# Kernel optimization log

Measured on AMD Instinct MI355X. Metric: run time of the kernel, lower is better.

The kernel has to match this reference:

```python
import jax, jax.numpy as jnp
import numpy as np

N, D_IN, D_OUT = 500000, 128, 128
DROP_P = 0.5


def setup_inputs() -> dict:
    key = jax.random.key(0)
    k1, k2, k3, k4 = jax.random.split(key, 4)
    x = jax.random.normal(k1, (N, D_IN), dtype=jnp.float32)
    weight = jax.random.normal(k2, (D_IN, D_OUT), dtype=jnp.float32)
    support = jax.random.normal(k3, (D_OUT, D_OUT), dtype=jnp.float32)
    # inverted-dropout mask: Bernoulli(keep=1-p) scaled by 1/(1-p), matching F.dropout in training mode
    keep = 1.0 - DROP_P
    u = jax.random.uniform(k4, (N, D_IN), dtype=jnp.float32)
    drop_mask = (u < keep).astype(jnp.float32) / keep
    return {"x": x, "weight": weight, "support": support, "drop_mask": drop_mask}


def reference(x, weight, support, drop_mask):
    # training-mode dropout (deterministic mask), dense transform, right-multiply by support, ReLU
    xd = x * drop_mask                      # [N, D_IN]
    xw = jnp.matmul(xd, weight)             # [N, D_OUT]
    out = jnp.matmul(xw, support)           # [N, D_OUT]
    return jax.nn.relu(out)
```

## Files before the change

kernel.cpp:

```cpp
#include <hip/hip_runtime.h>
#include <hip/hip_bf16.h>


#define D 128
#define LDS_PITCH 136

typedef __attribute__((ext_vector_type(8))) short short8;
typedef __attribute__((ext_vector_type(4))) float f32x4;

__device__ __forceinline__ short f2bf(float f) {
    union { __hip_bfloat16 h; short s; } u;
    u.h = __float2bfloat16(f);
    return u.s;
}

__global__ void wprod_kernel(const float* __restrict__ weight,
                             const float* __restrict__ support,
                             unsigned short* __restrict__ wt) {
    __shared__ float wrow[D];
    const int i = blockIdx.x;
    const int j = threadIdx.x;
    wrow[j] = weight[i * D + j];
    __syncthreads();
    float acc = 0.f;
#pragma unroll 8
    for (int k = 0; k < D; ++k)
        acc = fmaf(wrow[k], support[k * D + j], acc);
    union { __hip_bfloat16 h; unsigned short s; } u;
    u.h = __float2bfloat16(acc);
    wt[(size_t)j * D + i] = u.s;
}

__global__ __launch_bounds__(256, 4) void gcn_fused(
    const float* __restrict__ x, const float* __restrict__ mask,
    const unsigned short* __restrict__ wt, float* __restrict__ out,
    int nslabs) {
    __shared__ __align__(16) unsigned short lw[D * LDS_PITCH];

    const uint4* src = reinterpret_cast<const uint4*>(wt);
    for (int c = threadIdx.x; c < 2048; c += 256) {
        const int n = c >> 4;
        const int kc = (c & 15) << 3;
        *reinterpret_cast<uint4*>(&lw[n * LDS_PITCH + kc]) = src[c];
    }
    __syncthreads();

    const int lane = threadIdx.x & 63;
    const int m = lane & 15;
    const int quad = lane >> 4;

    const int wave = (blockIdx.x * blockDim.x + threadIdx.x) >> 6;
    const int nwaves = (gridDim.x * blockDim.x) >> 6;

    for (int s = wave; s < nslabs; s += nwaves) {
        const float* xr = x + ((size_t)s * 16 + m) * D + quad * 8;
        const float* mr = mask + ((size_t)s * 16 + m) * D + quad * 8;

        short8 a[4];
#pragma unroll
        for (int kk = 0; kk < 4; ++kk) {
            f32x4 x0 = *reinterpret_cast<const f32x4*>(xr + kk * 32);
            f32x4 x1 = *reinterpret_cast<const f32x4*>(xr + kk * 32 + 4);
            f32x4 m0 = *reinterpret_cast<const f32x4*>(mr + kk * 32);
            f32x4 m1 = *reinterpret_cast<const f32x4*>(mr + kk * 32 + 4);
            f32x4 p0 = x0 * m0;
            f32x4 p1 = x1 * m1;
            short8 v;
            v[0] = f2bf(p0[0]); v[1] = f2bf(p0[1]);
            v[2] = f2bf(p0[2]); v[3] = f2bf(p0[3]);
            v[4] = f2bf(p1[0]); v[5] = f2bf(p1[1]);
            v[6] = f2bf(p1[2]); v[7] = f2bf(p1[3]);
            a[kk] = v;
        }

        float* orow = out + (size_t)s * 16 * D;
#pragma unroll
        for (int n = 0; n < 8; ++n) {
            f32x4 acc = {0.f, 0.f, 0.f, 0.f};
#pragma unroll
            for (int kk = 0; kk < 4; ++kk) {
                const short8 b = *reinterpret_cast<const short8*>(
                    &lw[(n * 16 + m) * LDS_PITCH + kk * 32 + quad * 8]);
                acc = __builtin_amdgcn_mfma_f32_16x16x32_bf16(a[kk], b, acc, 0, 0, 0);
            }
#pragma unroll
            for (int r = 0; r < 4; ++r) {
                const float v = acc[r];
                orow[(quad * 4 + r) * D + n * 16 + m] = v > 0.f ? v : 0.f;
            }
        }
    }
}

extern "C" void kernel_launch(void* const* d_in, const int* in_sizes, int n_in,
                              void* d_out, int out_size, void* d_ws, size_t ws_size,
                              hipStream_t stream) {
    const float* x = (const float*)d_in[0];
    const float* weight = (const float*)d_in[1];
    const float* support = (const float*)d_in[2];
    const float* mask = (const float*)d_in[3];
    float* out = (float*)d_out;
    unsigned short* wt = (unsigned short*)d_ws;

    const int nrows = in_sizes[0] / D;
    const int nslabs = nrows / 16;

    wprod_kernel<<<dim3(D), dim3(D), 0, stream>>>(weight, support, wt);
    gcn_fused<<<dim3(2048), dim3(256), 0, stream>>>(x, mask, wt, out, nslabs);
}
```

Before: 645.1 us.

## Prefetch next slab, swap MFMA operands for vector stores, XOR-swizzle LDS

The loads of x and mask for the next 16-row slab are now issued before the MFMA work on the current slab, so global-memory latency is hidden behind compute. The MFMA operands are swapped so each lane holds four consecutive output columns, letting it write a single 16-byte store in place of four scattered scalar stores. LDS padding is replaced by an XOR swizzle to avoid bank conflicts, and the grid is halved so each wave handles more slabs. The prefetch doubles the registers held for x and mask, which may reduce occupancy.

```diff
diff --git a/kernel.cpp b/kernel.cpp
--- a/kernel.cpp
+++ b/kernel.cpp
@@ -3,7 +3,6 @@
 
 
 #define D 128
-#define LDS_PITCH 136
 
 typedef __attribute__((ext_vector_type(8))) short short8;
 typedef __attribute__((ext_vector_type(4))) float f32x4;
@@ -35,36 +34,49 @@
     const float* __restrict__ x, const float* __restrict__ mask,
     const unsigned short* __restrict__ wt, float* __restrict__ out,
     int nslabs) {
-    __shared__ __align__(16) unsigned short lw[D * LDS_PITCH];
+    __shared__ __align__(16) unsigned short lw[D * D];
 
     const uint4* src = reinterpret_cast<const uint4*>(wt);
     for (int c = threadIdx.x; c < 2048; c += 256) {
         const int n = c >> 4;
-        const int kc = (c & 15) << 3;
-        *reinterpret_cast<uint4*>(&lw[n * LDS_PITCH + kc]) = src[c];
+        const int gs = (c & 15) ^ (n & 7);
+        *reinterpret_cast<uint4*>(&lw[(n << 7) + (gs << 3)]) = src[c];
     }
     __syncthreads();
 
     const int lane = threadIdx.x & 63;
     const int m = lane & 15;
     const int quad = lane >> 4;
+    const int mx = m & 7;
 
-    const int wave = (blockIdx.x * blockDim.x + threadIdx.x) >> 6;
-    const int nwaves = (gridDim.x * blockDim.x) >> 6;
+    const int wave = (int)((blockIdx.x * blockDim.x + threadIdx.x) >> 6);
+    const int nwaves = (int)((gridDim.x * blockDim.x) >> 6);
 
-    for (int s = wave; s < nslabs; s += nwaves) {
-        const float* xr = x + ((size_t)s * 16 + m) * D + quad * 8;
-        const float* mr = mask + ((size_t)s * 16 + m) * D + quad * 8;
+    const int rowoff = m * D + quad * 8;
 
+    int s = wave;
+    if (s >= nslabs) return;
+
+    f32x4 vx[8], vm[8];
+
+    {
+        const float* xr = x + (size_t)s * (16 * D) + rowoff;
+        const float* mr = mask + (size_t)s * (16 * D) + rowoff;
+#pragma unroll
+        for (int kk = 0; kk < 4; ++kk) {
+            vx[2 * kk]     = *reinterpret_cast<const f32x4*>(xr + kk * 32);
+            vx[2 * kk + 1] = *reinterpret_cast<const f32x4*>(xr + kk * 32 + 4);
+            vm[2 * kk]     = *reinterpret_cast<const f32x4*>(mr + kk * 32);
+            vm[2 * kk + 1] = *reinterpret_cast<const f32x4*>(mr + kk * 32 + 4);
+        }
+    }
+
+    while (true) {
         short8 a[4];
 #pragma unroll
         for (int kk = 0; kk < 4; ++kk) {
-            f32x4 x0 = *reinterpret_cast<const f32x4*>(xr + kk * 32);
-            f32x4 x1 = *reinterpret_cast<const f32x4*>(xr + kk * 32 + 4);
-            f32x4 m0 = *reinterpret_cast<const f32x4*>(mr + kk * 32);
-            f32x4 m1 = *reinterpret_cast<const f32x4*>(mr + kk * 32 + 4);
-            f32x4 p0 = x0 * m0;
-            f32x4 p1 = x1 * m1;
+            f32x4 p0 = vx[2 * kk] * vm[2 * kk];
+            f32x4 p1 = vx[2 * kk + 1] * vm[2 * kk + 1];
             short8 v;
             v[0] = f2bf(p0[0]); v[1] = f2bf(p0[1]);
             v[2] = f2bf(p0[2]); v[3] = f2bf(p0[3]);
@@ -73,22 +85,38 @@
             a[kk] = v;
         }
 
-        float* orow = out + (size_t)s * 16 * D;
+        const int snext = s + nwaves;
+        const bool more = snext < nslabs;
+        if (more) {
+            const float* xr = x + (size_t)snext * (16 * D) + rowoff;
+            const float* mr = mask + (size_t)snext * (16 * D) + rowoff;
+#pragma unroll
+            for (int kk = 0; kk < 4; ++kk) {
+                vx[2 * kk]     = *reinterpret_cast<const f32x4*>(xr + kk * 32);
+                vx[2 * kk + 1] = *reinterpret_cast<const f32x4*>(xr + kk * 32 + 4);
+                vm[2 * kk]     = *reinterpret_cast<const f32x4*>(mr + kk * 32);
+                vm[2 * kk + 1] = *reinterpret_cast<const f32x4*>(mr + kk * 32 + 4);
+            }
+        }
+
+        float* orow = out + (size_t)s * (16 * D) + m * D;
 #pragma unroll
         for (int n = 0; n < 8; ++n) {
             f32x4 acc = {0.f, 0.f, 0.f, 0.f};
 #pragma unroll
             for (int kk = 0; kk < 4; ++kk) {
                 const short8 b = *reinterpret_cast<const short8*>(
-                    &lw[(n * 16 + m) * LDS_PITCH + kk * 32 + quad * 8]);
-                acc = __builtin_amdgcn_mfma_f32_16x16x32_bf16(a[kk], b, acc, 0, 0, 0);
+                    &lw[(((n << 4) + m) << 7) + ((((kk << 2) + quad) ^ mx) << 3)]);
+                acc = __builtin_amdgcn_mfma_f32_16x16x32_bf16(b, a[kk], acc, 0, 0, 0);
             }
+            f32x4 rv;
 #pragma unroll
-            for (int r = 0; r < 4; ++r) {
-                const float v = acc[r];
-                orow[(quad * 4 + r) * D + n * 16 + m] = v > 0.f ? v : 0.f;
-            }
+            for (int r = 0; r < 4; ++r) rv[r] = acc[r] > 0.f ? acc[r] : 0.f;
+            *reinterpret_cast<f32x4*>(&orow[(n << 4) + (quad << 2)]) = rv;
         }
+
+        if (!more) break;
+        s = snext;
     }
 }
 
@@ -106,5 +134,5 @@
     const int nslabs = nrows / 16;
 
     wprod_kernel<<<dim3(D), dim3(D), 0, stream>>>(weight, support, wt);
-    gcn_fused<<<dim3(2048), dim3(256), 0, stream>>>(x, mask, wt, out, nslabs);
+    gcn_fused<<<dim3(1024), dim3(256), 0, stream>>>(x, mask, wt, out, nslabs);
 }
```

Measured after the change: 772.1 us. 1.2x slower.
